# Optimization experiments

Measured on AMD Instinct MI355X. Metric: run time of the kernel, lower is better.

## Reference

```python
import jax, jax.numpy as jnp
import numpy as np

SCALE = 1.0 / np.sqrt(512.0).astype(np.float32)  # attention() hardcodes d_k=512


def setup_inputs() -> dict:
    key = jax.random.key(0)
    ks = jax.random.split(key, 9)
    B, S, D = 4, 2048, 512
    mk = lambda k, shape: jax.random.normal(k, shape, dtype=jnp.float32) * 0.05
    return {
        "q": mk(ks[0], (B, S, D)),
        "k": mk(ks[1], (B, S, D)),
        "v": mk(ks[2], (B, S, D)),
        "WQ_w": mk(ks[3], (D, D)),
        "WQ_b": mk(ks[4], (D,)),
        "WK_w": mk(ks[5], (D, D)),
        "WK_b": mk(ks[6], (D,)),
        "WV_w": mk(ks[7], (D, D)),
        "WV_b": mk(ks[8], (D,)),
    }


def reference(q, k, v, WQ_w, WQ_b, WK_w, WK_b, WV_w, WV_b):
    # torch nn.Linear: y = x @ W.T + b
    qp = q @ WQ_w.T + WQ_b  # [B,S,dk]
    kp = k @ WK_w.T + WK_b  # [B,S,dk]
    vp = v @ WV_w.T + WV_b  # [B,S,dv]
    qk = jnp.einsum("bqd,bkd->bqk", qp, kp) * SCALE  # [B,Sq,Sk]
    S = qk.shape[1]
    tril = jnp.tril(jnp.ones((S, S), dtype=qk.dtype))  # multiplicative causal mask
    qk = qk * tril
    # NOTE: original applies softmax over dim=1 (the query axis), faithfully kept.
    attn = jax.nn.softmax(qk, axis=1)
    out = jnp.einsum("bqk,bkd->bqd", attn, vp)  # [B,Sq,dv]
    return out
```

## Files before the change

kernel.cpp:

```cpp
#include <hip/hip_runtime.h>
#include <hip/hip_bf16.h>


#define S_LEN 2048
#define D_DIM 512
#define SCALE_F 0.044194173824159216f

typedef __attribute__((ext_vector_type(8))) short s8v;
typedef __attribute__((ext_vector_type(4))) short s4v;
typedef __attribute__((ext_vector_type(4))) float f4v;

enum { EPI_BIAS = 0, EPI_BIAS_T = 1, EPI_SCORES = 2 };

#define SBAR()    __builtin_amdgcn_s_barrier()
#define SCHEDB()  __builtin_amdgcn_sched_barrier(0)
#define WAITV(n)  asm volatile("s_waitcnt vmcnt(" #n ")")
#define WAITL0()  asm volatile("s_waitcnt lgkmcnt(0)")

__device__ __forceinline__ short f2bf_s(float f) {
  union { __hip_bfloat16 b; short s; } u; u.b = __float2bfloat16(f); return u.s;
}
__device__ __forceinline__ float bf2f_s(short h) {
  union { short s; __hip_bfloat16 b; } u; u.s = h; return __bfloat162float(u.b);
}

__device__ __forceinline__ void glds16(const short* g, short* l) {
  __builtin_amdgcn_global_load_lds((const __attribute__((address_space(1))) void*)g,
                                   (__attribute__((address_space(3))) void*)l, 16, 0, 0);
}

__device__ __forceinline__ unsigned lds_addr(const short* p) {
  return (unsigned)(unsigned long long)(const __attribute__((address_space(3))) short*)p;
}

__device__ __forceinline__ s8v dsr128(unsigned a) {
  s8v r;
  asm volatile("ds_read_b128 %0, %1" : "=&v"(r) : "v"(a));
  return r;
}

template <int EPI>
__device__ __forceinline__ void gemm_core512(
    const short* __restrict__ A, const short* __restrict__ B,
    short* __restrict__ C, const float* __restrict__ bias,
    short* SMEM, int N, size_t sCz, int m0, int n0, int bz,
    float* __restrict__ Z)
{
  const int tid  = threadIdx.x;
  const int w    = tid >> 6;
  const int lane = tid & 63;
  const int quad = lane >> 4;
  const int l16  = lane & 15;
  const int wm   = (w >> 1) * 64;
  const int wn   = (w & 1) * 64;

  const int strow = tid >> 3;
  const int gl = ((tid & 7) ^ (strow & 7)) * 8;

  f4v acc[4][4];
#pragma unroll
  for (int i = 0; i < 4; ++i)
#pragma unroll
    for (int j = 0; j < 4; ++j)
#pragma unroll
      for (int r = 0; r < 4; ++r) acc[i][j][r] = 0.0f;

  const short* Ag = A + (size_t)(m0 + strow) * 512 + gl;
  const short* Bg = B + (size_t)(n0 + strow) * 512 + gl;
  const size_t pstr = (size_t)32 * 512;
  const int t8 = tid * 8;
  const int swq = l16 & 7;

  const unsigned base = lds_addr(SMEM);
  unsigned aoff[4], boff[4];
#pragma unroll
  for (int ii = 0; ii < 4; ++ii)
    aoff[ii] = base + (unsigned)((wm + ii * 16 + l16) * 128 + ((quad ^ swq) * 16));
#pragma unroll
  for (int j = 0; j < 4; ++j)
    boff[j] = base + 16384u + (unsigned)((wn + j * 16 + l16) * 128 + ((quad ^ swq) * 16));

#define STAGE512(kt, b)                                                        \
  {                                                                            \
    short* dst_ = SMEM + (b) * 16384 + t8;                                     \
    const int ko_ = (kt) << 6;                                                 \
    _Pragma("unroll")                                                          \
    for (int p = 0; p < 4; ++p) glds16(Ag + ko_ + p * pstr, dst_ + p * 2048);  \
    _Pragma("unroll")                                                          \
    for (int p = 0; p < 4; ++p) glds16(Bg + ko_ + p * pstr, dst_ + 8192 + p * 2048); \
  }

  STAGE512(0, 0);
  STAGE512(1, 1);
  STAGE512(2, 2);

  for (int kt = 0; kt < 8; ++kt) {
    if (kt <= 5)      { WAITV(16); }
    else if (kt == 6) { WAITV(8);  }
    else              { WAITV(0);  }
    SBAR();
    SCHEDB();

    if (kt < 5) STAGE512(kt + 3, (kt + 3) & 3);

    const unsigned cofs = (unsigned)((kt & 3) * 32768);
#pragma unroll
    for (int kk = 0; kk < 2; ++kk) {
      const unsigned kx = (unsigned)(kk << 6);
      s8v af[4], bf[4];
#pragma unroll
      for (int ii = 0; ii < 4; ++ii) af[ii] = dsr128((aoff[ii] ^ kx) + cofs);
#pragma unroll
      for (int j = 0; j < 4; ++j)   bf[j]  = dsr128((boff[j] ^ kx) + cofs);
      WAITL0();
      SCHEDB();
      __builtin_amdgcn_s_setprio(1);
#pragma unroll
      for (int ii = 0; ii < 4; ++ii)
#pragma unroll
        for (int j = 0; j < 4; ++j)
          acc[ii][j] = __builtin_amdgcn_mfma_f32_16x16x32_bf16(af[ii], bf[j], acc[ii][j], 0, 0, 0);
      __builtin_amdgcn_s_setprio(0);
    }
  }
#undef STAGE512

  float bv[4];
  if (EPI == EPI_BIAS || EPI == EPI_BIAS_T) {
#pragma unroll
    for (int j = 0; j < 4; ++j) bv[j] = bias[n0 + wn + j * 16 + l16];
  }

  if (EPI == EPI_BIAS_T) {
#pragma unroll
    for (int i = 0; i < 4; ++i) {
#pragma unroll
      for (int j = 0; j < 4; ++j) {
        const int gn  = n0 + wn + j * 16 + l16;
        const int gmb = m0 + wm + i * 16 + quad * 4;
        const int bb = gmb >> 11, ssb = gmb & (S_LEN - 1);
        s4v o;
#pragma unroll
        for (int r = 0; r < 4; ++r) o[r] = f2bf_s(acc[i][j][r] + bv[j]);
        *(s4v*)&C[((size_t)bb * D_DIM + gn) * S_LEN + ssb] = o;
      }
    }
    return;
  }

  short* TB = SMEM;
  const int wbase = w * 2176;
  float csum[4] = {0.f, 0.f, 0.f, 0.f};

#pragma unroll
  for (int ph = 0; ph < 2; ++ph) {
    __syncthreads();
#pragma unroll
    for (int ii = 0; ii < 2; ++ii) {
      const int i = ph * 2 + ii;
#pragma unroll
      for (int j = 0; j < 4; ++j) {
        const int gn = n0 + wn + j * 16 + l16;
#pragma unroll
        for (int r = 0; r < 4; ++r) {
          short o;
          if (EPI == EPI_SCORES) {
            const int gm = m0 + wm + i * 16 + quad * 4 + r;
            const float f = (gm >= gn) ? (__expf(acc[i][j][r] * SCALE_F) - 1.0f) : 0.0f;
            csum[j] += f;
            o = f2bf_s(f);
          } else {
            o = f2bf_s(acc[i][j][r] + bv[j]);
          }
          TB[wbase + (ii * 16 + quad * 4 + r) * 68 + j * 16 + l16] = o;
        }
      }
    }
    __syncthreads();
#pragma unroll
    for (int p = 0; p < 4; ++p) {
      const int row = p * 8 + (lane >> 3);
      const int cg  = lane & 7;
      const s8v vv = *(const s8v*)&TB[wbase + row * 68 + cg * 8];
      const int gm = m0 + wm + ph * 32 + row;
      const int gn = n0 + wn + cg * 8;
      *(s8v*)&C[sCz + (size_t)gm * N + gn] = vv;
    }
  }

  if (EPI == EPI_SCORES) {
#pragma unroll
    for (int j = 0; j < 4; ++j) {
      float cs = csum[j];
      cs += __shfl_xor(cs, 16, 64);
      cs += __shfl_xor(cs, 32, 64);
      if (quad == 0) atomicAdd(&Z[(bz << 11) + n0 + wn + j * 16 + l16], cs);
    }
  }
}

__global__ __launch_bounds__(256, 1) void gemm_scoresF(
    const short* __restrict__ A, const short* __restrict__ B, short* __restrict__ C,
    float* __restrict__ Z)
{
  __shared__ __align__(16) short SMEM[65536];
  const int bid = blockIdx.x;
  const int bsw = (bid & 7) * 68 + (bid >> 3);
  const int bz  = bsw / 136;
  const int t   = bsw - bz * 136;
  int ti = (int)((sqrtf(8.0f * t + 1.0f) - 1.0f) * 0.5f);
  while ((ti + 1) * (ti + 2) / 2 <= t) ++ti;
  while (ti * (ti + 1) / 2 > t) --ti;
  const int tj = t - ti * (ti + 1) / 2;
  gemm_core512<EPI_SCORES>(A + (size_t)bz * S_LEN * D_DIM, B + (size_t)bz * S_LEN * D_DIM,
                           C, nullptr, SMEM, S_LEN,
                           (size_t)bz * S_LEN * S_LEN, ti * 128, tj * 128, bz, Z);
}

__global__ __launch_bounds__(256, 1) void proj3(
    const short* __restrict__ a0, const short* __restrict__ a1, const short* __restrict__ a2,
    const short* __restrict__ b0, const short* __restrict__ b1, const short* __restrict__ b2,
    short* __restrict__ c0, short* __restrict__ c1, short* __restrict__ c2,
    const float* __restrict__ x0, const float* __restrict__ x1, const float* __restrict__ x2)
{
  __shared__ __align__(16) short SMEM[65536];
  const int bid = blockIdx.x;
  const int bsw = (bid & 7) * 96 + (bid >> 3);
  const int z   = bsw >> 8;
  const int rem = bsw & 255;
  const int m0  = (rem >> 2) * 128;
  const int n0  = (rem & 3) * 128;
  const short* A = (z == 0) ? a0 : (z == 1) ? a1 : a2;
  const short* B = (z == 0) ? b0 : (z == 1) ? b1 : b2;
  short*       C = (z == 0) ? c0 : (z == 1) ? c1 : c2;
  const float* bias = (z == 0) ? x0 : (z == 1) ? x1 : x2;
  if (z == 2)
    gemm_core512<EPI_BIAS_T>(A, B, C, bias, SMEM, D_DIM, 0, m0, n0, 0, nullptr);
  else
    gemm_core512<EPI_BIAS>(A, B, C, bias, SMEM, D_DIM, 0, m0, n0, 0, nullptr);
}

__global__ __launch_bounds__(256, 2) void gemm_outF(
    const short* __restrict__ F, const short* __restrict__ vpT,
    const float* __restrict__ Tv, float* __restrict__ out)
{
  __shared__ __align__(16) short SMEM[36864];

  const int tid  = threadIdx.x;
  const int h    = blockIdx.x;
  const int x    = h & 7;
  const int s    = h >> 3;
  const int n0   = (s & 3) * 128;
  const int bz   = (s >> 2) & 3;
  const int zslot = s >> 4;
  const int zs   = (zslot < 2) ? (2 * x + zslot) : (16 + 2 * x + (zslot - 2));
  const int mi   = (zs < 16) ? (31 - zs) : (zs - 16);
  const int m0   = mi * 64;

  const short* A = F   + (size_t)bz * S_LEN * S_LEN;
  const short* B = vpT + (size_t)bz * D_DIM * S_LEN;

  const int w    = tid >> 6;
  const int lane = tid & 63;
  const int quad = lane >> 4;
  const int l16  = lane & 15;
  const int wm   = (w >> 1) * 32;
  const int wn   = (w & 1) * 64;

  const int strow = tid >> 3;
  const int gl = ((tid & 7) ^ (strow & 7)) * 8;

  f4v acc[2][4];
#pragma unroll
  for (int i = 0; i < 2; ++i)
#pragma unroll
    for (int j = 0; j < 4; ++j)
#pragma unroll
      for (int r = 0; r < 4; ++r) acc[i][j][r] = 0.0f;

  const short* Ag = A + (size_t)(m0 + strow) * S_LEN + gl;
  const short* Bg = B + (size_t)(n0 + strow) * S_LEN + gl;
  const size_t pstr = (size_t)32 * S_LEN;
  const int t8 = tid * 8;
  const int swq = l16 & 7;

  const unsigned base = lds_addr(SMEM);
  unsigned aoff[2], boff[4];
#pragma unroll
  for (int ii = 0; ii < 2; ++ii)
    aoff[ii] = base + (unsigned)((wm + ii * 16 + l16) * 128 + ((quad ^ swq) * 16));
#pragma unroll
  for (int j = 0; j < 4; ++j)
    boff[j] = base + 8192u + (unsigned)((wn + j * 16 + l16) * 128 + ((quad ^ swq) * 16));

  const int niter = mi + 1;

#pragma unroll
  for (int pre = 0; pre < 2; ++pre) {
    short* dst = SMEM + pre * 12288 + t8;
    const int k0 = pre << 6;
#pragma unroll
    for (int p = 0; p < 2; ++p) glds16(Ag + k0 + p * pstr, dst + p * 2048);
#pragma unroll
    for (int p = 0; p < 4; ++p) glds16(Bg + k0 + p * pstr, dst + 4096 + p * 2048);
  }

  int cbuf = 0;
  for (int i = 0; i < niter; ++i) {
    if (i + 1 < niter) { WAITV(6); } else { WAITV(0); }
    SBAR();
    SCHEDB();

    if (i + 2 < niter) {
      int nb = cbuf + 2; if (nb >= 3) nb -= 3;
      const int k2 = (i + 2) << 6;
      short* dst = SMEM + nb * 12288 + t8;
#pragma unroll
      for (int p = 0; p < 2; ++p) glds16(Ag + k2 + p * pstr, dst + p * 2048);
#pragma unroll
      for (int p = 0; p < 4; ++p) glds16(Bg + k2 + p * pstr, dst + 4096 + p * 2048);
      SCHEDB();
    }

    const unsigned cofs = (unsigned)(cbuf * 24576);
    cbuf = (cbuf == 2) ? 0 : cbuf + 1;
#pragma unroll
    for (int kk = 0; kk < 2; ++kk) {
      const unsigned kx = (unsigned)(kk << 6);
      s8v af[2], bf[4];
#pragma unroll
      for (int ii = 0; ii < 2; ++ii) af[ii] = dsr128((aoff[ii] ^ kx) + cofs);
#pragma unroll
      for (int j = 0; j < 4; ++j)   bf[j]  = dsr128((boff[j] ^ kx) + cofs);
      WAITL0();
      SCHEDB();
      __builtin_amdgcn_s_setprio(1);
#pragma unroll
      for (int ii = 0; ii < 2; ++ii)
#pragma unroll
        for (int j = 0; j < 4; ++j)
          acc[ii][j] = __builtin_amdgcn_mfma_f32_16x16x32_bf16(af[ii], bf[j], acc[ii][j], 0, 0, 0);
      __builtin_amdgcn_s_setprio(0);
    }
  }

  float* Cf = out + (size_t)bz * S_LEN * D_DIM;
#pragma unroll
  for (int i = 0; i < 2; ++i) {
#pragma unroll
    for (int j = 0; j < 4; ++j) {
      const int gn = n0 + wn + j * 16 + l16;
      const float tvn = Tv[(bz << 9) + gn];
#pragma unroll
      for (int r = 0; r < 4; ++r) {
        const int gm = m0 + wm + i * 16 + quad * 4 + r;
        Cf[(size_t)gm * D_DIM + gn] = acc[i][j][r] + tvn;
      }
    }
  }
}

__global__ __launch_bounds__(256) void cvt_all(
    const float* __restrict__ q, const float* __restrict__ k, const float* __restrict__ v,
    const float* __restrict__ wq, const float* __restrict__ wk, const float* __restrict__ wv,
    short* __restrict__ qb, short* __restrict__ Wqb)
{
  const int y = blockIdx.y;
  const float* s; short* d; int i;
  if (blockIdx.x < 2048) {
    s = (y == 0) ? q : (y == 1) ? k : v;
    d = qb + (size_t)y * 4194304;
    i = (blockIdx.x * 256 + threadIdx.x) * 8;
  } else {
    s = (y == 0) ? wq : (y == 1) ? wk : wv;
    d = Wqb + (size_t)y * 262144;
    i = ((int)(blockIdx.x - 2048) * 256 + threadIdx.x) * 8;
  }
  const float4 f0 = *(const float4*)(s + i);
  const float4 f1 = *(const float4*)(s + i + 4);
  s8v o;
  o[0] = f2bf_s(f0.x); o[1] = f2bf_s(f0.y); o[2] = f2bf_s(f0.z); o[3] = f2bf_s(f0.w);
  o[4] = f2bf_s(f1.x); o[5] = f2bf_s(f1.y); o[6] = f2bf_s(f1.z); o[7] = f2bf_s(f1.w);
  *(s8v*)(d + i) = o;
}

__global__ __launch_bounds__(256) void scale_vpt_T(
    short* __restrict__ vpT, const float* __restrict__ ZF, float* __restrict__ Tv)
{
  __shared__ float red[4];
  const int b = blockIdx.y, d = blockIdx.x, tid = threadIdx.x;
  const size_t rowbase = ((size_t)(b * D_DIM + d)) * S_LEN;
  const float* zf = ZF + (b << 11);
  const int k0 = tid * 8;

  s8v v = *(s8v*)&vpT[rowbase + k0];
  float s = 0.0f;
#pragma unroll
  for (int i = 0; i < 8; ++i) {
    const float w = bf2f_s(v[i]) / (2048.0f + zf[k0 + i]);
    s += w;
    v[i] = f2bf_s(w);
  }
  *(s8v*)&vpT[rowbase + k0] = v;

#pragma unroll
  for (int off = 32; off >= 1; off >>= 1) s += __shfl_xor(s, off, 64);
  if ((tid & 63) == 0) red[tid >> 6] = s;
  __syncthreads();
  if (tid == 0) Tv[(b << 9) + d] = red[0] + red[1] + red[2] + red[3];
}

extern "C" void kernel_launch(void* const* d_in, const int* in_sizes, int n_in,
                              void* d_out, int out_size, void* d_ws, size_t ws_size,
                              hipStream_t stream) {
  const float* q   = (const float*)d_in[0];
  const float* k   = (const float*)d_in[1];
  const float* v   = (const float*)d_in[2];
  const float* WQw = (const float*)d_in[3];
  const float* WQb = (const float*)d_in[4];
  const float* WKw = (const float*)d_in[5];
  const float* WKb = (const float*)d_in[6];
  const float* WVw = (const float*)d_in[7];
  const float* WVb = (const float*)d_in[8];

  char* ws = (char*)d_ws;
  short* F   = (short*)(ws);
  short* qb  = (short*)(ws);
  short* Wqb = (short*)(ws + 25165824);
  short* qp  = (short*)(ws + 33554432);
  short* kp  = (short*)(ws + 41943040);
  short* vpT = (short*)(ws + 50331648);
  float* ZF  = (float*)(ws + 58720256);
  float* Tv  = (float*)(ws + 58753024);
  short* kb  = qb + 4194304;
  short* vb  = qb + 8388608;
  short* Wkb = Wqb + 262144;
  short* Wvb = Wqb + 524288;

  const dim3 blk(256);

  (void)hipMemsetAsync(ZF, 0, 4 * S_LEN * sizeof(float), stream);

  cvt_all<<<dim3(2176, 3), blk, 0, stream>>>(q, k, v, WQw, WKw, WVw, qb, Wqb);

  proj3<<<dim3(768), blk, 0, stream>>>(
      qb, kb, vb, Wqb, Wkb, Wvb, qp, kp, vpT, WQb, WKb, WVb);

  gemm_scoresF<<<dim3(544), blk, 0, stream>>>(qp, kp, F, ZF);

  scale_vpt_T<<<dim3(512, 4), blk, 0, stream>>>(vpT, ZF, Tv);

  gemm_outF<<<dim3(512), blk, 0, stream>>>(F, vpT, Tv, (float*)d_out);
}
```

Before: 177.9 us.

## Load B fragments directly from global, shrink LDS to allow three blocks per CU

The 128x128x512 GEMM core no longer stages the B operand through LDS. Each wave now reads its B MFMA fragments directly from global memory into registers, and only A is double-buffered in LDS (two stages instead of a four-deep pipeline holding both A and B). This cuts LDS use from 128KB to 32KB per block, and launch bounds are raised to 3 blocks per CU for the scores and projection kernels to gain occupancy. The output kernel's block-to-tile mapping is also simplified. The trade-off is uncoalesced global reads of B and a shallower prefetch pipeline, which may expose memory latency.

```diff
diff --git a/kernel.cpp b/kernel.cpp
--- a/kernel.cpp
+++ b/kernel.cpp
@@ -66,52 +66,56 @@
       for (int r = 0; r < 4; ++r) acc[i][j][r] = 0.0f;
 
   const short* Ag = A + (size_t)(m0 + strow) * 512 + gl;
-  const short* Bg = B + (size_t)(n0 + strow) * 512 + gl;
   const size_t pstr = (size_t)32 * 512;
   const int t8 = tid * 8;
   const int swq = l16 & 7;
 
+  const short* Bf = B + (size_t)(n0 + wn + l16) * 512 + (quad << 3);
+
   const unsigned base = lds_addr(SMEM);
-  unsigned aoff[4], boff[4];
+  unsigned aoff[4];
 #pragma unroll
   for (int ii = 0; ii < 4; ++ii)
     aoff[ii] = base + (unsigned)((wm + ii * 16 + l16) * 128 + ((quad ^ swq) * 16));
-#pragma unroll
-  for (int j = 0; j < 4; ++j)
-    boff[j] = base + 16384u + (unsigned)((wn + j * 16 + l16) * 128 + ((quad ^ swq) * 16));
-
-#define STAGE512(kt, b)                                                        \
+
+#define STAGEA(kt, b)                                                          \
   {                                                                            \
-    short* dst_ = SMEM + (b) * 16384 + t8;                                     \
+    short* dst_ = SMEM + (b) * 8192 + t8;                                      \
     const int ko_ = (kt) << 6;                                                 \
     _Pragma("unroll")                                                          \
     for (int p = 0; p < 4; ++p) glds16(Ag + ko_ + p * pstr, dst_ + p * 2048);  \
-    _Pragma("unroll")                                                          \
-    for (int p = 0; p < 4; ++p) glds16(Bg + ko_ + p * pstr, dst_ + 8192 + p * 2048); \
-  }
-
-  STAGE512(0, 0);
-  STAGE512(1, 1);
-  STAGE512(2, 2);
+  }
+
+  STAGEA(0, 0);
 
   for (int kt = 0; kt < 8; ++kt) {
-    if (kt <= 5)      { WAITV(16); }
-    else if (kt == 6) { WAITV(8);  }
-    else              { WAITV(0);  }
+    const int c = kt & 1;
+
+    s8v bcur[2][4];
+#pragma unroll
+    for (int kk = 0; kk < 2; ++kk)
+#pragma unroll
+      for (int j = 0; j < 4; ++j)
+        bcur[kk][j] = *(const s8v*)(Bf + j * (16 * 512) + (kt << 6) + (kk << 5));
+    SCHEDB();
+
+    if (kt < 7) {
+      STAGEA(kt + 1, 1 - c);
+      SCHEDB();
+      WAITV(12);
+    } else {
+      WAITV(8);
+    }
     SBAR();
     SCHEDB();
 
-    if (kt < 5) STAGE512(kt + 3, (kt + 3) & 3);
-
-    const unsigned cofs = (unsigned)((kt & 3) * 32768);
+    const unsigned cofs = (unsigned)(c << 14);
 #pragma unroll
     for (int kk = 0; kk < 2; ++kk) {
       const unsigned kx = (unsigned)(kk << 6);
-      s8v af[4], bf[4];
+      s8v af[4];
 #pragma unroll
       for (int ii = 0; ii < 4; ++ii) af[ii] = dsr128((aoff[ii] ^ kx) + cofs);
-#pragma unroll
-      for (int j = 0; j < 4; ++j)   bf[j]  = dsr128((boff[j] ^ kx) + cofs);
       WAITL0();
       SCHEDB();
       __builtin_amdgcn_s_setprio(1);
@@ -119,11 +123,11 @@
       for (int ii = 0; ii < 4; ++ii)
 #pragma unroll
         for (int j = 0; j < 4; ++j)
-          acc[ii][j] = __builtin_amdgcn_mfma_f32_16x16x32_bf16(af[ii], bf[j], acc[ii][j], 0, 0, 0);
+          acc[ii][j] = __builtin_amdgcn_mfma_f32_16x16x32_bf16(af[ii], bcur[kk][j], acc[ii][j], 0, 0, 0);
       __builtin_amdgcn_s_setprio(0);
     }
   }
-#undef STAGE512
+#undef STAGEA
 
   float bv[4];
   if (EPI == EPI_BIAS || EPI == EPI_BIAS_T) {
@@ -199,11 +203,11 @@
   }
 }
 
-__global__ __launch_bounds__(256, 1) void gemm_scoresF(
+__global__ __launch_bounds__(256, 3) void gemm_scoresF(
     const short* __restrict__ A, const short* __restrict__ B, short* __restrict__ C,
     float* __restrict__ Z)
 {
-  __shared__ __align__(16) short SMEM[65536];
+  __shared__ __align__(16) short SMEM[16384];
   const int bid = blockIdx.x;
   const int bsw = (bid & 7) * 68 + (bid >> 3);
   const int bz  = bsw / 136;
@@ -217,13 +221,13 @@
                            (size_t)bz * S_LEN * S_LEN, ti * 128, tj * 128, bz, Z);
 }
 
-__global__ __launch_bounds__(256, 1) void proj3(
+__global__ __launch_bounds__(256, 3) void proj3(
     const short* __restrict__ a0, const short* __restrict__ a1, const short* __restrict__ a2,
     const short* __restrict__ b0, const short* __restrict__ b1, const short* __restrict__ b2,
     short* __restrict__ c0, short* __restrict__ c1, short* __restrict__ c2,
     const float* __restrict__ x0, const float* __restrict__ x1, const float* __restrict__ x2)
 {
-  __shared__ __align__(16) short SMEM[65536];
+  __shared__ __align__(16) short SMEM[16384];
   const int bid = blockIdx.x;
   const int bsw = (bid & 7) * 96 + (bid >> 3);
   const int z   = bsw >> 8;
@@ -248,12 +252,9 @@
 
   const int tid  = threadIdx.x;
   const int h    = blockIdx.x;
-  const int x    = h & 7;
-  const int s    = h >> 3;
-  const int n0   = (s & 3) * 128;
-  const int bz   = (s >> 2) & 3;
-  const int zslot = s >> 4;
-  const int zs   = (zslot < 2) ? (2 * x + zslot) : (16 + 2 * x + (zslot - 2));
+  const int n0   = (h & 3) * 128;
+  const int bz   = (h >> 2) & 3;
+  const int zs   = h >> 4;
   const int mi   = (zs < 16) ? (31 - zs) : (zs - 16);
   const int m0   = mi * 64;
 
```

New measurement: 193.6 us. 1.09x slower.
